# Performance work log

Measured on AMD Instinct MI355X. Metric: run time of the kernel, lower is better.

Reference implementation:

```python
import jax, jax.numpy as jnp
from jax import lax
import numpy as np

N_ENT = 50000
N_REL = 500
E = 800000
H = 128
BS = 1024
C = 96
KER = 7
KH, KW = 8, 16  # H = KH*KW
TOPK = 15
FLAT = C * (2 * KH - KER + 1) * (KW - KER + 1)  # 96*10*10 = 9600


def mlp3(x, w0, b0, w1, b1, w2, b2):
    x = jax.nn.relu(x @ w0 + b0)
    x = jax.nn.relu(x @ w1 + b1)
    return x @ w2 + b2


def compute_corr(x1, x2):
    x1 = x1 - jnp.mean(x1, 0, keepdims=True)
    x2 = x2 - jnp.mean(x2, 0, keepdims=True)
    s1 = jnp.sqrt(jnp.mean(x1 * x1))
    s2 = jnp.sqrt(jnp.mean(x2 * x2))
    return jnp.abs(jnp.mean(x1 * x2)) / (s1 * s2)


def comp_layer(node_emb, rel_emb, src, dst, rel_id, neigh_w):
    # CompGCN 'mul' composition: u_mul_e
    comp = node_emb[src] * rel_emb[rel_id]                      # (E,H)
    score = jnp.sum(comp * node_emb[dst], axis=-1)              # e_dot_v, (E,)
    # edge softmax over incoming edges of each dst node
    m = jax.ops.segment_max(score, dst, num_segments=N_ENT)
    e = jnp.exp(score - m[dst])
    z = jax.ops.segment_sum(e, dst, num_segments=N_ENT)
    norm = e / z[dst]                                           # (E,)
    # select_topk: keep top-15 in-edges per dst by norm
    order = jnp.lexsort((-norm, dst))                           # sort by dst, then norm desc
    deg = jax.ops.segment_sum(jnp.ones((E,), jnp.int32), dst, num_segments=N_ENT)
    start = jnp.cumsum(deg) - deg                               # group start per node
    rank = jnp.arange(E, dtype=jnp.int32) - start[dst[order]]
    keep = jnp.zeros((E,), bool).at[order].set(rank < TOPK)
    w = norm * keep                                             # weighted, pruned
    # copy_e + sum aggregation to dst
    neigh = jax.ops.segment_sum(comp * w[:, None], dst, num_segments=N_ENT)
    return jnp.tanh(neigh @ neigh_w)


def conve(head, rel, ent_emb, conv_w, conv_b, fc_w, fc_b, score_b):
    x = jnp.concatenate([head.reshape(-1, 1, KH, KW), rel.reshape(-1, 1, KH, KW)], axis=2)  # (bs,1,16,16)
    x = lax.conv_general_dilated(x, conv_w, (1, 1), 'VALID') + conv_b[None, :, None, None]
    x = jax.nn.relu(x).reshape(x.shape[0], -1)                  # (bs,FLAT)
    x = jax.nn.relu(x @ fc_w + fc_b)                            # (bs,H)
    return jax.nn.sigmoid(x @ ent_emb.T + score_b)              # (bs,N_ENT)


def setup_inputs() -> dict:
    key = jax.random.key(0)
    ks = jax.random.split(key, 24)
    def g(i, shape, scale=0.05):
        return jax.random.normal(ks[i], shape, jnp.float32) * scale
    return dict(
        h_id=jax.random.randint(ks[0], (BS,), 0, N_ENT),
        r_id=jax.random.randint(ks[1], (BS,), 0, 2 * N_REL),
        src=jax.random.randint(ks[2], (E,), 0, N_ENT),
        dst=jax.random.randint(ks[3], (E,), 0, N_ENT),
        rel_id=jax.random.randint(ks[4], (E,), 0, 2 * N_REL),
        ent_emb=g(5, (N_ENT, H)),
        rel_emb0=g(6, (2 * N_REL, H)),
        neigh_w=g(7, (H, H)),
        S_w=g(8, (H, H)), S_b=jnp.zeros((H,), jnp.float32),
        L_w=g(9, (H, H)), L_b=jnp.zeros((H,), jnp.float32),
        pred_rel_emb=g(10, (2 * N_REL, H)),
        phi_w0=g(11, (H, 200)), phi_b0=jnp.zeros((200,), jnp.float32),
        phi_w1=g(12, (200, 200)), phi_b1=jnp.zeros((200,), jnp.float32),
        phi_w2=g(13, (200, 1)), phi_b2=jnp.zeros((1,), jnp.float32),
        psi_w0=g(14, (H, 200)), psi_b0=jnp.zeros((200,), jnp.float32),
        psi_w1=g(15, (200, 200)), psi_b1=jnp.zeros((200,), jnp.float32),
        psi_w2=g(16, (200, 1)), psi_b2=jnp.zeros((1,), jnp.float32),
        conv_w=g(17, (C, 1, KER, KER)), conv_b=jnp.zeros((C,), jnp.float32),
        fc_w=g(18, (FLAT, H)), fc_b=jnp.zeros((H,), jnp.float32),
        score_b=jnp.zeros((N_ENT,), jnp.float32),
    )


def reference(h_id, r_id, src, dst, rel_id,
              ent_emb, rel_emb0, neigh_w, S_w, S_b, L_w, L_b, pred_rel_emb,
              phi_w0, phi_b0, phi_w1, phi_b1, phi_w2, phi_b2,
              psi_w0, psi_b0, psi_w1, psi_b1, psi_w2, psi_b2,
              conv_w, conv_b, fc_w, fc_b, score_b):
    common = ent_emb @ S_w + S_b
    private = ent_emb @ L_w + L_b
    c1 = comp_layer(common, rel_emb0, src, dst, rel_id, neigh_w)
    c2 = comp_layer(private, rel_emb0, src, dst, rel_id, neigh_w)
    ent_out = ent_emb + c1 + c2
    corr = compute_corr(mlp3(c1, phi_w0, phi_b0, phi_w1, phi_b1, phi_w2, phi_b2),
                        mlp3(c2, psi_w0, psi_b0, psi_w1, psi_b1, psi_w2, psi_b2))
    head = ent_out[h_id]
    rel = pred_rel_emb[r_id]
    score = conve(head, rel, ent_out, conv_w, conv_b, fc_w, fc_b, score_b)
    return (score, corr)
```

## Files before the change

### kernel.cpp

```cpp
#include <hip/hip_runtime.h>
#include <math.h>

typedef unsigned short ushort;
typedef unsigned int   uint;
typedef short bf16x8 __attribute__((ext_vector_type(8)));
typedef float f32x4  __attribute__((ext_vector_type(4)));
typedef ushort u16x8 __attribute__((ext_vector_type(8)));
typedef ushort u16x4 __attribute__((ext_vector_type(4)));

#define N_ENTS   50000
#define E_EDGES  800000
#define HD       128
#define BSZ      1024
#define C_CH     96
#define FLATD    9600
#define TOPK_K   15
#define HIDD     200
#define SPLITK   10
#define OUT_SCORE ((size_t)BSZ * N_ENTS)

#define MPAD     50048
#define NPAD_ENT 50176
#define KPAD200  224
#define NPAD200  256
#define L2E      1.4426950408889634f

#define OFF_EP       ((size_t)0)
#define OFF_ENTOUT   ((size_t)25624576)
#define OFF_RELBF    ((size_t)38469632)
#define OFF_PRELBF   ((size_t)38725632)
#define OFF_SWT      ((size_t)38981632)
#define OFF_LWT      ((size_t)39014400)
#define OFF_NWT      ((size_t)39047168)
#define OFF_P0T      ((size_t)39079936)
#define OFF_Q0T      ((size_t)39145472)
#define OFF_P1T      ((size_t)39211008)
#define OFF_Q1T      ((size_t)39325696)
#define OFF_FCT      ((size_t)39440384)
#define OFF_SC       ((size_t)41897984)
#define OFF_W        ((size_t)48297984)
#define OFF_SIDX     ((size_t)54697984)
#define OFF_EORD     ((size_t)67497984)
#define OFF_DEG      ((size_t)70697984)
#define OFF_START    ((size_t)70897984)
#define OFF_CUR      ((size_t)71097984)
#define OFF_BSUM     ((size_t)71297984)
#define OFF_X1       ((size_t)71302080)
#define OFF_X2       ((size_t)71502080)
#define OFF_RED      ((size_t)71702080)
#define OFF_XFC      ((size_t)71702336)
#define OFF_ARENA    ((size_t)71964480)

__device__ inline ushort f2b(float f) {
    uint u = __float_as_uint(f);
    return (ushort)((u + 0x7fffu + ((u >> 16) & 1u)) >> 16);
}
__device__ inline float b2f(ushort u) { return __uint_as_float((uint)u << 16); }
__device__ inline float fexp2(float x) { return __builtin_amdgcn_exp2f(x); }
__device__ inline float frcp(float x)  { return __builtin_amdgcn_rcpf(x); }
__device__ inline float fsigmoid(float x) { return frcp(1.f + fexp2(-x * L2E)); }
__device__ inline float ftanh(float x) {
    float ax = fabsf(x);
    float t = fexp2(ax * (-2.f * L2E));
    float r = (1.f - t) * frcp(1.f + t);
    return copysignf(r, x);
}

__global__ void k_cvt(const float* __restrict__ in, ushort* __restrict__ out,
                      int M, int Mpad, int K) {
    int i = blockIdx.x * 256 + threadIdx.x;
    if (i >= Mpad * K) return;
    int r = i / K;
    out[i] = (r < M) ? f2b(in[i]) : (ushort)0;
}

__global__ void k_cvt2(const float* __restrict__ in0, ushort* __restrict__ out0,
                       const float* __restrict__ in1, ushort* __restrict__ out1, int n) {
    const float* in = blockIdx.z ? in1 : in0;
    ushort* out = blockIdx.z ? out1 : out0;
    int i = blockIdx.x * 256 + threadIdx.x;
    if (i < n) out[i] = f2b(in[i]);
}

__global__ __launch_bounds__(256) void k_tcvtT(const float* __restrict__ in, ushort* __restrict__ out,
                                               int K, int N, int Kpad, int Npad) {
    __shared__ float t[32][33];
    int k0 = blockIdx.x * 32, n0 = blockIdx.y * 32;
    int tx = threadIdx.x & 31, ty = threadIdx.x >> 5;
    for (int i = ty; i < 32; i += 8) {
        int k = k0 + i, n = n0 + tx;
        t[i][tx] = (k < K && n < N) ? in[(size_t)k * N + n] : 0.f;
    }
    __syncthreads();
    for (int i = ty; i < 32; i += 8) {
        int n = n0 + i, k = k0 + tx;
        if (n < Npad && k < Kpad) out[(size_t)n * Kpad + k] = f2b(t[tx][i]);
    }
}

__global__ __launch_bounds__(256) void k_tcvt7(
    const float* __restrict__ S_w, const float* __restrict__ L_w, const float* __restrict__ n_w,
    const float* __restrict__ p0, const float* __restrict__ q0,
    const float* __restrict__ p1, const float* __restrict__ q1,
    ushort* __restrict__ Swt, ushort* __restrict__ Lwt, ushort* __restrict__ nWt,
    ushort* __restrict__ p0t, ushort* __restrict__ q0t,
    ushort* __restrict__ p1t, ushort* __restrict__ q1t) {
    const float* in; ushort* out; int K, N, Kp, Np;
    switch (blockIdx.z) {
        case 0: in = S_w; out = Swt; K = 128; N = 128; Kp = 128; Np = 128; break;
        case 1: in = L_w; out = Lwt; K = 128; N = 128; Kp = 128; Np = 128; break;
        case 2: in = n_w; out = nWt; K = 128; N = 128; Kp = 128; Np = 128; break;
        case 3: in = p0;  out = p0t; K = 128; N = HIDD; Kp = 128; Np = NPAD200; break;
        case 4: in = q0;  out = q0t; K = 128; N = HIDD; Kp = 128; Np = NPAD200; break;
        case 5: in = p1;  out = p1t; K = HIDD; N = HIDD; Kp = KPAD200; Np = NPAD200; break;
        default: in = q1; out = q1t; K = HIDD; N = HIDD; Kp = KPAD200; Np = NPAD200; break;
    }
    __shared__ float t[32][33];
    int k0 = blockIdx.x * 32, n0 = blockIdx.y * 32;
    if (k0 >= Kp || n0 >= Np) return;
    int tx = threadIdx.x & 31, ty = threadIdx.x >> 5;
    for (int i = ty; i < 32; i += 8) {
        int k = k0 + i, n = n0 + tx;
        t[i][tx] = (k < K && n < N) ? in[(size_t)k * N + n] : 0.f;
    }
    __syncthreads();
    for (int i = ty; i < 32; i += 8) {
        int n = n0 + i, k = k0 + tx;
        if (n < Np && k < Kp) out[(size_t)n * Kp + k] = f2b(t[tx][i]);
    }
}

template <int WM, int WN, int OUTBF, int FUSE2>
__global__ __launch_bounds__(256) void k_mgemm(
    const ushort* __restrict__ A, int lda,
    const ushort* __restrict__ Bt, int ldb,
    const float* __restrict__ bias, void* __restrict__ Cout, int ldc,
    int M, int N, int K, int kChunk, int epi, int iofs, int npad,
    const ushort* __restrict__ A2, const ushort* __restrict__ Bt2,
    const float* __restrict__ bias2, void* __restrict__ Cout2, int iofs2) {
    if (FUSE2 && blockIdx.z == 1) { A = A2; Bt = Bt2; bias = bias2; Cout = Cout2; iofs = iofs2; }
    const int w = threadIdx.x >> 6, lane = threadIdx.x & 63;
    const int wr = w / WN, wc = w % WN;
    const int row0 = blockIdx.x * (WM * 64) + wr * 64;
    const int col0 = blockIdx.y * (WN * 64) + wc * 64;
    const int lr = lane & 15;
    const int kg = (lane >> 4) * 8;
    const int kb = FUSE2 ? 0 : blockIdx.z * kChunk;
    const int ke = kb + kChunk;

    f32x4 acc[4][4];
#pragma unroll
    for (int i = 0; i < 4; i++)
#pragma unroll
        for (int j = 0; j < 4; j++) acc[i][j] = (f32x4){0.f, 0.f, 0.f, 0.f};

    for (int kk = kb; kk < ke; kk += 32) {
        bf16x8 af[4], bfr[4];
#pragma unroll
        for (int i = 0; i < 4; i++) {
            int r = row0 + i * 16 + lr;
            r = min(r, M - 1);
            af[i] = *(const bf16x8*)(A + (size_t)r * lda + kk + kg);
        }
#pragma unroll
        for (int j = 0; j < 4; j++) {
            int c = col0 + j * 16 + lr;
            bfr[j] = *(const bf16x8*)(Bt + (size_t)c * ldb + kk + kg);
        }
#pragma unroll
        for (int i = 0; i < 4; i++)
#pragma unroll
            for (int j = 0; j < 4; j++)
                acc[i][j] = __builtin_amdgcn_mfma_f32_16x16x32_bf16(af[i], bfr[j], acc[i][j], 0, 0, 0);
    }

    const int cr = (lane >> 4) * 4, cc = lane & 15;
    if (!FUSE2 && gridDim.z > 1) {
        float* P = (float*)Cout + (size_t)blockIdx.z * M * ldc;
#pragma unroll
        for (int i = 0; i < 4; i++)
#pragma unroll
            for (int j = 0; j < 4; j++) {
                int col = col0 + j * 16 + cc;
                if (col >= N) continue;
#pragma unroll
                for (int t = 0; t < 4; t++) {
                    int row = row0 + i * 16 + cr + t;
                    if (row < M) P[(size_t)row * ldc + col] = acc[i][j][t];
                }
            }
    } else {
#pragma unroll
        for (int i = 0; i < 4; i++)
#pragma unroll
            for (int j = 0; j < 4; j++) {
                int col = col0 + j * 16 + cc;
                if (col >= (OUTBF ? npad : N)) continue;
                bool valid = col < N;
                float bi = (bias && valid) ? bias[col] : 0.f;
#pragma unroll
                for (int t = 0; t < 4; t++) {
                    int row = row0 + i * 16 + cr + t;
                    if (row >= M) continue;
                    float v = acc[i][j][t] + bi;
                    if (epi == 1) v = fmaxf(v, 0.f);
                    else if (epi == 2) v = ftanh(v);
                    else if (epi == 3) v = fsigmoid(v);
                    if (!valid) v = 0.f;
                    if (OUTBF) {
                        size_t idx = (iofs < 0) ? ((size_t)row * ldc + col)
                                   : ((size_t)row * ldc + ((size_t)(col >> 1) << 2) + (col & 1) + iofs);
                        ((ushort*)Cout)[idx] = f2b(v);
                    } else {
                        ((float*)Cout)[(size_t)row * ldc + col] = v;
                    }
                }
            }
    }
}

__global__ __launch_bounds__(256) void k_score(
    const ushort* __restrict__ A,
    const ushort* __restrict__ Bt,
    const float* __restrict__ bias,
    float* __restrict__ C, int N) {
    __shared__ __align__(16) float st[4][16][68];
    const int w = threadIdx.x >> 6, lane = threadIdx.x & 63;
    const int lr = lane & 15, kg = (lane >> 4) * 8;
    const int cr = (lane >> 4) * 4, cc = lane & 15;
    int flat = blockIdx.y * 16 + blockIdx.x;
    int swz = (flat & 7) * 392 + (flat >> 3);
    const int row0 = (swz & 15) * 64;
    const int colw = (swz >> 4) * 256 + w * 64;

    f32x4 acc[4][4];
#pragma unroll
    for (int i = 0; i < 4; i++)
#pragma unroll
        for (int j = 0; j < 4; j++) acc[i][j] = (f32x4){0.f, 0.f, 0.f, 0.f};

    for (int kk = 0; kk < HD; kk += 32) {
        bf16x8 af[4], bfr[4];
#pragma unroll
        for (int i = 0; i < 4; i++)
            af[i] = *(const bf16x8*)(A + (size_t)(row0 + i * 16 + lr) * HD + kk + kg);
#pragma unroll
        for (int j = 0; j < 4; j++)
            bfr[j] = *(const bf16x8*)(Bt + (size_t)(colw + j * 16 + lr) * HD + kk + kg);
#pragma unroll
        for (int i = 0; i < 4; i++)
#pragma unroll
            for (int j = 0; j < 4; j++)
                acc[i][j] = __builtin_amdgcn_mfma_f32_16x16x32_bf16(af[i], bfr[j], acc[i][j], 0, 0, 0);
    }

#pragma unroll
    for (int i = 0; i < 4; i++) {
#pragma unroll
        for (int j = 0; j < 4; j++) {
            int col = colw + j * 16 + cc;
            float bi = (col < N) ? bias[col] : 0.f;
#pragma unroll
            for (int t = 0; t < 4; t++)
                st[w][cr + t][j * 16 + cc] = fsigmoid(acc[i][j][t] + bi);
        }
#pragma unroll
        for (int p = 0; p < 4; p++) {
            int r = p * 4 + (lane >> 4);
            int cq = (lane & 15) * 4;
            float4 v = *(const float4*)&st[w][r][cq];
            int gc = colw + cq;
            if (gc < N)
                *(float4*)&C[(size_t)(row0 + i * 16 + r) * N + gc] = v;
        }
    }
}

__global__ __launch_bounds__(256) void k_mlp2(
    const ushort* __restrict__ A0, const ushort* __restrict__ W0t0,
    const float* __restrict__ b00, const ushort* __restrict__ W1t0,
    const float* __restrict__ b10, const float* __restrict__ w20,
    const float* __restrict__ b20, float* __restrict__ xo0,
    const ushort* __restrict__ A1, const ushort* __restrict__ W0t1,
    const float* __restrict__ b01, const ushort* __restrict__ W1t1,
    const float* __restrict__ b11, const float* __restrict__ w21,
    const float* __restrict__ b21, float* __restrict__ xo1) {
    const ushort* A   = blockIdx.z ? A1 : A0;
    const ushort* W0t = blockIdx.z ? W0t1 : W0t0;
    const float*  b0  = blockIdx.z ? b01 : b00;
    const ushort* W1t = blockIdx.z ? W1t1 : W1t0;
    const float*  b1  = blockIdx.z ? b11 : b10;
    const float*  w2  = blockIdx.z ? w21 : w20;
    const float*  b2  = blockIdx.z ? b21 : b20;
    float*        x   = blockIdx.z ? xo1 : xo0;

    __shared__ __align__(16) char lbuf[64 * 232 * 2];
    __shared__ float w2e[256], b1e[256], b0e[256];
    const int tid = threadIdx.x;
    const int w = tid >> 6, lane = tid & 63;
    const int lr = lane & 15, kg = (lane >> 4) * 8;
    const int cr = (lane >> 4) * 4, cc = lane & 15;
    const int row0 = blockIdx.x * 64;
    {
        int c = tid;
        w2e[c] = (c < HIDD) ? w2[c] : 0.f;
        b1e[c] = (c < HIDD) ? b1[c] : 0.f;
        b0e[c] = (c < HIDD) ? b0[c] : 0.f;
    }
    __syncthreads();
    ushort* g1 = (ushort*)lbuf;

    f32x4 acc[4][4];
#pragma unroll
    for (int i = 0; i < 4; i++)
#pragma unroll
        for (int j = 0; j < 4; j++) acc[i][j] = (f32x4){0.f, 0.f, 0.f, 0.f};
    for (int kk = 0; kk < 128; kk += 32) {
        bf16x8 af[4], bfr[4];
#pragma unroll
        for (int i = 0; i < 4; i++)
            af[i] = *(const bf16x8*)(A + (size_t)(row0 + i * 16 + lr) * HD + kk + kg);
#pragma unroll
        for (int j = 0; j < 4; j++)
            bfr[j] = *(const bf16x8*)(W0t + (size_t)(w * 64 + j * 16 + lr) * 128 + kk + kg);
#pragma unroll
        for (int i = 0; i < 4; i++)
#pragma unroll
            for (int j = 0; j < 4; j++)
                acc[i][j] = __builtin_amdgcn_mfma_f32_16x16x32_bf16(af[i], bfr[j], acc[i][j], 0, 0, 0);
    }
#pragma unroll
    for (int i = 0; i < 4; i++)
#pragma unroll
        for (int j = 0; j < 4; j++) {
            int col = w * 64 + j * 16 + cc;
            if (col < KPAD200) {
                float bi = b0e[col];
#pragma unroll
                for (int t = 0; t < 4; t++)
                    g1[(i * 16 + cr + t) * 232 + col] = f2b(fmaxf(acc[i][j][t] + bi, 0.f));
            }
        }
    __syncthreads();

    f32x4 a2[4][4];
#pragma unroll
    for (int i = 0; i < 4; i++)
#pragma unroll
        for (int j = 0; j < 4; j++) a2[i][j] = (f32x4){0.f, 0.f, 0.f, 0.f};
    for (int ks = 0; ks < 7; ks++) {
        int kk = ks * 32;
        bf16x8 af[4], bfr[4];
#pragma unroll
        for (int i = 0; i < 4; i++)
            af[i] = *(const bf16x8*)(g1 + (i * 16 + lr) * 232 + kk + kg);
#pragma unroll
        for (int j = 0; j < 4; j++)
            bfr[j] = *(const bf16x8*)(W1t + (size_t)(w * 64 + j * 16 + lr) * KPAD200 + kk + kg);
#pragma unroll
        for (int i = 0; i < 4; i++)
#pragma unroll
            for (int j = 0; j < 4; j++)
                a2[i][j] = __builtin_amdgcn_mfma_f32_16x16x32_bf16(af[i], bfr[j], a2[i][j], 0, 0, 0);
    }
    __syncthreads();

    float* pbuf = (float*)lbuf;
#pragma unroll
    for (int i = 0; i < 4; i++)
#pragma unroll
        for (int t = 0; t < 4; t++) {
            float s = 0.f;
#pragma unroll
            for (int j = 0; j < 4; j++) {
                int col = w * 64 + j * 16 + cc;
                s += fmaxf(a2[i][j][t] + b1e[col], 0.f) * w2e[col];
            }
            pbuf[(i * 16 + cr + t) * 65 + w * 16 + cc] = s;
        }
    __syncthreads();
    if (tid < 64) {
        float s = b2[0];
        for (int q = 0; q < 64; q++) s += pbuf[tid * 65 + q];
        int gr = row0 + tid;
        if (gr < N_ENTS) x[gr] = s;
    }
}

__global__ void k_deg(const int* __restrict__ dst, int* __restrict__ deg) {
    int e = blockIdx.x * 256 + threadIdx.x;
    if (e < E_EDGES) atomicAdd(&deg[dst[e]], 1);
}

__global__ void k_scan1(const int* __restrict__ in, int* __restrict__ out,
                        int* __restrict__ bsum, int n) {
    __shared__ int sh[256];
    int i = blockIdx.x * 256 + threadIdx.x;
    int v = (i < n) ? in[i] : 0;
    sh[threadIdx.x] = v; __syncthreads();
    for (int off = 1; off < 256; off <<= 1) {
        int t = (threadIdx.x >= off) ? sh[threadIdx.x - off] : 0;
        __syncthreads();
        sh[threadIdx.x] += t;
        __syncthreads();
    }
    if (i < n) out[i] = sh[threadIdx.x] - v;
    if (threadIdx.x == 255) bsum[blockIdx.x] = sh[255];
}

__global__ void k_scan2(int* __restrict__ bsum, int nb) {
    __shared__ int sh[1024];
    int t = threadIdx.x;
    int v = (t < nb) ? bsum[t] : 0;
    sh[t] = v; __syncthreads();
    for (int off = 1; off < 1024; off <<= 1) {
        int u = (t >= off) ? sh[t - off] : 0;
        __syncthreads();
        sh[t] += u;
        __syncthreads();
    }
    if (t < nb) bsum[t] = sh[t] - v;
}

__global__ void k_scan3(int* __restrict__ out, const int* __restrict__ bsum, int n) {
    int i = blockIdx.x * 256 + threadIdx.x;
    if (i < n) out[i] += bsum[blockIdx.x];
}

__global__ void k_scatter(const int* __restrict__ dst, const int* __restrict__ start,
                          int* __restrict__ cursor, int* __restrict__ eorder) {
    int e = blockIdx.x * 256 + threadIdx.x;
    if (e < E_EDGES) {
        int n = dst[e];
        int p = start[n] + atomicAdd(&cursor[n], 1);
        eorder[p] = e;
    }
}

__global__ void k_mkidx(const int* __restrict__ eorder, const int* __restrict__ src,
                        const int* __restrict__ dst, const int* __restrict__ rel_id,
                        int4* __restrict__ sidx) {
    int slot = blockIdx.x * 256 + threadIdx.x;
    if (slot < E_EDGES) {
        int e = eorder[slot];
        sidx[slot] = make_int4(src[e], dst[e], rel_id[e], e);
    }
}

__global__ __launch_bounds__(256) void k_scores(
    const int4* __restrict__ sidx, const ushort* __restrict__ ep,
    const ushort* __restrict__ rel, float2* __restrict__ sc) {
    int gg = threadIdx.x >> 3, l = threadIdx.x & 7;
    int slot = blockIdx.x * 32 + gg;
    int4 si = sidx[slot];
    const ushort* rs = ep + (size_t)si.x * 256 + l * 32;
    const ushort* rd = ep + (size_t)si.y * 256 + l * 32;
    const ushort* rr = rel + (size_t)si.z * 128 + l * 16;
    u16x8 sv[4], dv[4], rv[2];
#pragma unroll
    for (int i = 0; i < 4; i++) sv[i] = *(const u16x8*)(rs + 8 * i);
#pragma unroll
    for (int i = 0; i < 4; i++) dv[i] = *(const u16x8*)(rd + 8 * i);
#pragma unroll
    for (int i = 0; i < 2; i++) rv[i] = *(const u16x8*)(rr + 8 * i);
    float a = 0.f, b = 0.f;
#pragma unroll
    for (int Q = 0; Q < 8; Q++) {
        int G = Q >> 1, k = (Q & 1) * 4;
        float r0 = b2f(rv[Q >> 2][(Q & 3) * 2]);
        float r1 = b2f(rv[Q >> 2][(Q & 3) * 2 + 1]);
        a += b2f(sv[G][k])     * r0 * b2f(dv[G][k])     + b2f(sv[G][k + 1]) * r1 * b2f(dv[G][k + 1]);
        b += b2f(sv[G][k + 2]) * r0 * b2f(dv[G][k + 2]) + b2f(sv[G][k + 3]) * r1 * b2f(dv[G][k + 3]);
    }
#pragma unroll
    for (int m = 4; m; m >>= 1) { a += __shfl_xor(a, m, 8); b += __shfl_xor(b, m, 8); }
    if (l == 0) sc[slot] = make_float2(a, b);
}

__global__ __launch_bounds__(256) void k_softtop(
    const int* __restrict__ start, const int* __restrict__ deg,
    const int4* __restrict__ sidx, const float2* __restrict__ sc, float2* __restrict__ w) {
    int n = blockIdx.x * 16 + (threadIdx.x >> 4);
    int l = threadIdx.x & 15;
    if (n >= N_ENTS) return;
    int b = start[n], d = deg[n];
    if (d == 0) return;
    float m1 = -INFINITY, m2 = -INFINITY;
    for (int i = l; i < d; i += 16) {
        float2 s = sc[b + i];
        m1 = fmaxf(m1, s.x); m2 = fmaxf(m2, s.y);
    }
#pragma unroll
    for (int o = 8; o; o >>= 1) { m1 = fmaxf(m1, __shfl_xor(m1, o, 16)); m2 = fmaxf(m2, __shfl_xor(m2, o, 16)); }
    float z1 = 0.f, z2 = 0.f;
    for (int i = l; i < d; i += 16) {
        float2 s = sc[b + i];
        z1 += fexp2((s.x - m1) * L2E); z2 += fexp2((s.y - m2) * L2E);
    }
#pragma unroll
    for (int o = 8; o; o >>= 1) { z1 += __shfl_xor(z1, o, 16); z2 += __shfl_xor(z2, o, 16); }
    float iz1 = frcp(z1), iz2 = frcp(z2);
    for (int i = l; i < d; i += 16) {
        float2 sp = sc[b + i];
        int ei = sidx[b + i].w;
        int r1 = 0, r2 = 0;
        for (int j = 0; j < d; j++) {
            float2 sq = sc[b + j];
            int ej = sidx[b + j].w;
            r1 += (sq.x > sp.x) || (sq.x == sp.x && ej < ei);
            r2 += (sq.y > sp.y) || (sq.y == sp.y && ej < ei);
        }
        w[b + i] = make_float2(r1 < TOPK_K ? fexp2((sp.x - m1) * L2E) * iz1 : 0.f,
                               r2 < TOPK_K ? fexp2((sp.y - m2) * L2E) * iz2 : 0.f);
    }
}

__global__ __launch_bounds__(256) void k_agg(
    const int4* __restrict__ sidx, const int* __restrict__ start, const int* __restrict__ deg,
    const float2* __restrict__ w, const ushort* __restrict__ ep, const ushort* __restrict__ rel,
    ushort* __restrict__ neigh1, ushort* __restrict__ neigh2) {
    __shared__ float4 part[3][64];
    int n = blockIdx.x;
    int wid = threadIdx.x >> 6, g = threadIdx.x & 63;
    int b = start[n], end = b + deg[n];
    float2 a1 = make_float2(0.f, 0.f), a2 = make_float2(0.f, 0.f);
    float2 c1 = make_float2(0.f, 0.f), c2 = make_float2(0.f, 0.f);
    for (int s = b + wid; s < end; s += 8) {
        int sB = s + 4;
        bool hB = sB < end;
        int4 siA = sidx[s];
        float2 wA = w[s];
        int4 siB = hB ? sidx[sB] : siA;
        float2 wB = hB ? w[sB] : make_float2(0.f, 0.f);
        u16x4 vA = *(const u16x4*)(ep + (size_t)siA.x * 256 + g * 4);
        uint  rA = *(const uint*)(rel + (size_t)siA.z * 128 + g * 2);
        u16x4 vB = *(const u16x4*)(ep + (size_t)siB.x * 256 + g * 4);
        uint  rB = *(const uint*)(rel + (size_t)siB.z * 128 + g * 2);
        float rAx = b2f((ushort)(rA & 0xffffu)), rAy = b2f((ushort)(rA >> 16));
        a1.x += wA.x * b2f(vA[0]) * rAx;  a1.y += wA.x * b2f(vA[1]) * rAy;
        a2.x += wA.y * b2f(vA[2]) * rAx;  a2.y += wA.y * b2f(vA[3]) * rAy;
        float rBx = b2f((ushort)(rB & 0xffffu)), rBy = b2f((ushort)(rB >> 16));
        c1.x += wB.x * b2f(vB[0]) * rBx;  c1.y += wB.x * b2f(vB[1]) * rBy;
        c2.x += wB.y * b2f(vB[2]) * rBx;  c2.y += wB.y * b2f(vB[3]) * rBy;
    }
    a1.x += c1.x; a1.y += c1.y; a2.x += c2.x; a2.y += c2.y;
    if (wid > 0) part[wid - 1][g] = make_float4(a1.x, a1.y, a2.x, a2.y);
    __syncthreads();
    if (wid == 0) {
#pragma unroll
        for (int k = 0; k < 3; k++) {
            float4 p = part[k][g];
            a1.x += p.x; a1.y += p.y; a2.x += p.z; a2.y += p.w;
        }
        uint o1 = (uint)f2b(a1.x) | ((uint)f2b(a1.y) << 16);
        uint o2 = (uint)f2b(a2.x) | ((uint)f2b(a2.y) << 16);
        ((uint*)(neigh1 + (size_t)n * HD))[g] = o1;
        ((uint*)(neigh2 + (size_t)n * HD))[g] = o2;
    }
}

__global__ void k_entout(const float* __restrict__ ent, const ushort* __restrict__ c1,
                         const ushort* __restrict__ c2, ushort* __restrict__ out) {
    int i = blockIdx.x * 256 + threadIdx.x;
    if (i >= NPAD_ENT * HD) return;
    int r = i >> 7;
    float v = 0.f;
    if (r < N_ENTS) v = ent[i] + b2f(c1[i]) + b2f(c2[i]);
    out[i] = (r < N_ENTS) ? f2b(v) : (ushort)0;
}

__global__ void k_corr1(const float* __restrict__ x1, const float* __restrict__ x2,
                        float* __restrict__ red) {
    __shared__ float sa[1024], sb[1024];
    int t = threadIdx.x;
    float s1 = 0.f, s2 = 0.f;
    for (int i = t; i < N_ENTS; i += 1024) { s1 += x1[i]; s2 += x2[i]; }
    sa[t] = s1; sb[t] = s2; __syncthreads();
    for (int o = 512; o > 0; o >>= 1) {
        if (t < o) { sa[t] += sa[t + o]; sb[t] += sb[t + o]; }
        __syncthreads();
    }
    if (t == 0) { red[0] = sa[0] / (float)N_ENTS; red[1] = sb[0] / (float)N_ENTS; }
}

__global__ void k_corr2(const float* __restrict__ x1, const float* __restrict__ x2,
                        const float* __restrict__ red, float* __restrict__ out) {
    __shared__ float s11[1024], s22[1024], s12[1024];
    int t = threadIdx.x;
    float m1 = red[0], m2 = red[1];
    float a11 = 0.f, a22 = 0.f, a12 = 0.f;
    for (int i = t; i < N_ENTS; i += 1024) {
        float a = x1[i] - m1, b = x2[i] - m2;
        a11 += a * a; a22 += b * b; a12 += a * b;
    }
    s11[t] = a11; s22[t] = a22; s12[t] = a12; __syncthreads();
    for (int o = 512; o > 0; o >>= 1) {
        if (t < o) { s11[t] += s11[t + o]; s22[t] += s22[t + o]; s12[t] += s12[t + o]; }
        __syncthreads();
    }
    if (t == 0) {
        float v11 = s11[0] / (float)N_ENTS, v22 = s22[0] / (float)N_ENTS, v12 = s12[0] / (float)N_ENTS;
        out[0] = fabsf(v12) / (sqrtf(v11) * sqrtf(v22));
    }
}

__global__ void k_conv(const int* __restrict__ h_id, const int* __restrict__ r_id,
                       const ushort* __restrict__ entout, const ushort* __restrict__ prel,
                       const float* __restrict__ cw, const float* __restrict__ cb,
                       ushort* __restrict__ out) {
    __shared__ float img[256];
    __shared__ float filt[C_CH * 49];
    int b = blockIdx.x, tid = threadIdx.x;
    if (tid < 128) img[tid] = b2f(entout[(size_t)h_id[b] * HD + tid]);
    else           img[tid] = b2f(prel[(size_t)r_id[b] * HD + (tid - 128)]);
    for (int i = tid; i < C_CH * 49; i += 256) filt[i] = cw[i];
    __syncthreads();
    for (int idx = tid; idx < FLATD; idx += 256) {
        int o = idx / 100, rem = idx % 100, i = rem / 10, j = rem % 10;
        float acc = cb[o];
        const float* f = &filt[o * 49];
#pragma unroll
        for (int ki = 0; ki < 7; ki++)
#pragma unroll
            for (int kj = 0; kj < 7; kj++)
                acc += img[(i + ki) * 16 + (j + kj)] * f[ki * 7 + kj];
        out[(size_t)b * FLATD + idx] = f2b(fmaxf(acc, 0.f));
    }
}

__global__ void k_fcreduce(const float* __restrict__ part, const float* __restrict__ bias,
                           ushort* __restrict__ out) {
    int i = blockIdx.x * 256 + threadIdx.x;
    if (i >= BSZ * HD) return;
    float s = 0.f;
    for (int z = 0; z < SPLITK; z++) s += part[(size_t)z * BSZ * HD + i];
    s += bias[i & (HD - 1)];
    out[i] = f2b(fmaxf(s, 0.f));
}

extern "C" void kernel_launch(void* const* d_in, const int* in_sizes, int n_in,
                              void* d_out, int out_size, void* d_ws, size_t ws_size,
                              hipStream_t stream) {
    const int* h_id    = (const int*)d_in[0];
    const int* r_id    = (const int*)d_in[1];
    const int* src     = (const int*)d_in[2];
    const int* dst     = (const int*)d_in[3];
    const int* rel_id  = (const int*)d_in[4];
    const float* ent_emb  = (const float*)d_in[5];
    const float* rel_emb0 = (const float*)d_in[6];
    const float* neigh_w  = (const float*)d_in[7];
    const float* S_w = (const float*)d_in[8];
    const float* S_b = (const float*)d_in[9];
    const float* L_w = (const float*)d_in[10];
    const float* L_b = (const float*)d_in[11];
    const float* pred_rel = (const float*)d_in[12];
    const float* phi_w0 = (const float*)d_in[13]; const float* phi_b0 = (const float*)d_in[14];
    const float* phi_w1 = (const float*)d_in[15]; const float* phi_b1 = (const float*)d_in[16];
    const float* phi_w2 = (const float*)d_in[17]; const float* phi_b2 = (const float*)d_in[18];
    const float* psi_w0 = (const float*)d_in[19]; const float* psi_b0 = (const float*)d_in[20];
    const float* psi_w1 = (const float*)d_in[21]; const float* psi_b1 = (const float*)d_in[22];
    const float* psi_w2 = (const float*)d_in[23]; const float* psi_b2 = (const float*)d_in[24];
    const float* conv_w = (const float*)d_in[25]; const float* conv_b = (const float*)d_in[26];
    const float* fc_w   = (const float*)d_in[27]; const float* fc_b   = (const float*)d_in[28];
    const float* score_b= (const float*)d_in[29];

    char* base = (char*)d_ws;
    ushort* ep       = (ushort*)(base + OFF_EP);
    ushort* entout_bf= (ushort*)(base + OFF_ENTOUT);
    ushort* rel_bf   = (ushort*)(base + OFF_RELBF);
    ushort* prel_bf  = (ushort*)(base + OFF_PRELBF);
    ushort* Swt      = (ushort*)(base + OFF_SWT);
    ushort* Lwt      = (ushort*)(base + OFF_LWT);
    ushort* nWt      = (ushort*)(base + OFF_NWT);
    ushort* p0t      = (ushort*)(base + OFF_P0T);
    ushort* q0t      = (ushort*)(base + OFF_Q0T);
    ushort* p1t      = (ushort*)(base + OFF_P1T);
    ushort* q1t      = (ushort*)(base + OFF_Q1T);
    ushort* fct      = (ushort*)(base + OFF_FCT);
    float2* sc       = (float2*)(base + OFF_SC);
    float2* wpair    = (float2*)(base + OFF_W);
    int4*   sidx     = (int4*)(base + OFF_SIDX);
    int*    eorder   = (int*)(base + OFF_EORD);
    int*    deg      = (int*)(base + OFF_DEG);
    int*    startp   = (int*)(base + OFF_START);
    int*    cursor   = (int*)(base + OFF_CUR);
    int*    bsum     = (int*)(base + OFF_BSUM);
    float*  x1       = (float*)(base + OFF_X1);
    float*  x2       = (float*)(base + OFF_X2);
    float*  red      = (float*)(base + OFF_RED);
    ushort* xfc_bf   = (ushort*)(base + OFF_XFC);
    ushort* c1_bf    = (ushort*)(base + OFF_EP);
    ushort* c2_bf    = (ushort*)(base + OFF_EP + 12812288);
    ushort* ent_bf   = (ushort*)(base + OFF_ARENA);
    ushort* neigh1_bf= (ushort*)(base + OFF_ARENA);
    ushort* neigh2_bf= (ushort*)(base + OFF_ARENA + 12812288);
    ushort* convout  = (ushort*)(base + OFF_ARENA);
    float*  fcpart   = (float*)(base + OFF_ARENA + 22421504);
    float*  outf     = (float*)d_out;

    k_cvt<<<dim3((MPAD * HD + 255) / 256), 256, 0, stream>>>(ent_emb, ent_bf, N_ENTS, MPAD, HD);
    k_cvt2<<<dim3(500, 1, 2), 256, 0, stream>>>(rel_emb0, rel_bf, pred_rel, prel_bf, 1000 * HD);
    k_tcvt7<<<dim3(7, 8, 7), 256, 0, stream>>>(S_w, L_w, neigh_w, phi_w0, psi_w0, phi_w1, psi_w1,
                                               Swt, Lwt, nWt, p0t, q0t, p1t, q1t);
    k_tcvtT<<<dim3(300, 4), 256, 0, stream>>>(fc_w, fct, FLATD, 128, FLATD, 128);

    k_mgemm<2,2,1,1><<<dim3(391, 1, 2), 256, 0, stream>>>(
        ent_bf, HD, Swt, HD, S_b, ep, 256, N_ENTS, HD, HD, HD, 0, 0, HD,
        ent_bf, Lwt, L_b, ep, 2);

    hipMemsetAsync(deg, 0, N_ENTS * sizeof(int), stream);
    hipMemsetAsync(cursor, 0, N_ENTS * sizeof(int), stream);
    k_deg<<<dim3((E_EDGES + 255) / 256), 256, 0, stream>>>(dst, deg);
    int nscan = (N_ENTS + 255) / 256;
    k_scan1<<<dim3(nscan), 256, 0, stream>>>(deg, startp, bsum, N_ENTS);
    k_scan2<<<dim3(1), 1024, 0, stream>>>(bsum, nscan);
    k_scan3<<<dim3(nscan), 256, 0, stream>>>(startp, bsum, N_ENTS);
    k_scatter<<<dim3((E_EDGES + 255) / 256), 256, 0, stream>>>(dst, startp, cursor, eorder);
    k_mkidx<<<dim3((E_EDGES + 255) / 256), 256, 0, stream>>>(eorder, src, dst, rel_id, sidx);

    k_scores<<<dim3(E_EDGES / 32), 256, 0, stream>>>(sidx, ep, rel_bf, sc);
    k_softtop<<<dim3((N_ENTS + 15) / 16), 256, 0, stream>>>(startp, deg, sidx, sc, wpair);
    k_agg<<<dim3(N_ENTS), 256, 0, stream>>>(sidx, startp, deg, wpair, ep, rel_bf,
                                            neigh1_bf, neigh2_bf);

    k_mgemm<2,2,1,1><<<dim3(391, 1, 2), 256, 0, stream>>>(
        neigh1_bf, HD, nWt, HD, nullptr, c1_bf, HD, N_ENTS, HD, HD, HD, 2, -1, HD,
        neigh2_bf, nWt, nullptr, c2_bf, -1);

    k_entout<<<dim3((NPAD_ENT * HD + 255) / 256), 256, 0, stream>>>(ent_emb, c1_bf, c2_bf, entout_bf);

    k_mlp2<<<dim3(MPAD / 64, 1, 2), 256, 0, stream>>>(
        c1_bf, p0t, phi_b0, p1t, phi_b1, phi_w2, phi_b2, x1,
        c2_bf, q0t, psi_b0, q1t, psi_b1, psi_w2, psi_b2, x2);

    k_corr1<<<dim3(1), 1024, 0, stream>>>(x1, x2, red);
    k_corr2<<<dim3(1), 1024, 0, stream>>>(x1, x2, red, outf + OUT_SCORE);

    k_conv<<<dim3(BSZ), 256, 0, stream>>>(h_id, r_id, entout_bf, prel_bf, conv_w, conv_b, convout);
    k_mgemm<2,2,0,0><<<dim3(8, 1, SPLITK), 256, 0, stream>>>(
        convout, FLATD, fct, FLATD, nullptr, fcpart, HD, BSZ, HD, FLATD, FLATD / SPLITK, 0, -1, HD,
        nullptr, nullptr, nullptr, nullptr, 0);
    k_fcreduce<<<dim3((BSZ * HD + 255) / 256), 256, 0, stream>>>(fcpart, fc_b, xfc_bf);

    k_score<<<dim3(16, 196), 256, 0, stream>>>(xfc_bf, entout_bf, score_b, outf, N_ENTS);
}
```

Baseline: 699.4 us.

## Fuse neigh GEMM with ent_out, merge scatter/mkidx and corr kernels, tune agg

Several independent changes. The tanh GEMM for both branches is fused with the ent_out sum into one kernel, scatter and index building are merged, and the two corr kernels are combined, which removes launches and intermediate round-trips. k_score uses nontemporal stores for the large output, k_scores changes its load pattern, k_softtop skips top-k ranking for nodes with degree at most 15, and k_agg unrolls to four edges per iteration for more memory-level parallelism. entout padding rows beyond N_ENTS are no longer zeroed, which may matter if the score GEMM reads padded rows.

```diff
diff --git a/kernel.cpp b/kernel.cpp
--- a/kernel.cpp
+++ b/kernel.cpp
@@ -40,7 +40,6 @@
 #define OFF_SC       ((size_t)41897984)
 #define OFF_W        ((size_t)48297984)
 #define OFF_SIDX     ((size_t)54697984)
-#define OFF_EORD     ((size_t)67497984)
 #define OFF_DEG      ((size_t)70697984)
 #define OFF_START    ((size_t)70897984)
 #define OFF_CUR      ((size_t)71097984)
@@ -219,11 +218,65 @@
     }
 }
 
+__global__ __launch_bounds__(256) void k_tanh2ent(
+    const ushort* __restrict__ neigh1, const ushort* __restrict__ neigh2,
+    const ushort* __restrict__ nWt, const float* __restrict__ ent,
+    ushort* __restrict__ c1o, ushort* __restrict__ c2o, ushort* __restrict__ eo) {
+    const int w = threadIdx.x >> 6, lane = threadIdx.x & 63;
+    const int wr = w >> 1, wc = w & 1;
+    const int row0 = blockIdx.x * 128 + wr * 64;
+    const int col0 = wc * 64;
+    const int lr = lane & 15, kg = (lane >> 4) * 8;
+
+    f32x4 a1[4][4], a2[4][4];
+#pragma unroll
+    for (int i = 0; i < 4; i++)
+#pragma unroll
+        for (int j = 0; j < 4; j++) { a1[i][j] = (f32x4){0,0,0,0}; a2[i][j] = (f32x4){0,0,0,0}; }
+
+    for (int kk = 0; kk < HD; kk += 32) {
+        bf16x8 f1[4], f2v[4], bfr[4];
+#pragma unroll
+        for (int i = 0; i < 4; i++) {
+            int r = min(row0 + i * 16 + lr, N_ENTS - 1);
+            f1[i]  = *(const bf16x8*)(neigh1 + (size_t)r * HD + kk + kg);
+            f2v[i] = *(const bf16x8*)(neigh2 + (size_t)r * HD + kk + kg);
+        }
+#pragma unroll
+        for (int j = 0; j < 4; j++)
+            bfr[j] = *(const bf16x8*)(nWt + (size_t)(col0 + j * 16 + lr) * HD + kk + kg);
+#pragma unroll
+        for (int i = 0; i < 4; i++)
+#pragma unroll
+            for (int j = 0; j < 4; j++) {
+                a1[i][j] = __builtin_amdgcn_mfma_f32_16x16x32_bf16(f1[i],  bfr[j], a1[i][j], 0, 0, 0);
+                a2[i][j] = __builtin_amdgcn_mfma_f32_16x16x32_bf16(f2v[i], bfr[j], a2[i][j], 0, 0, 0);
+            }
+    }
+
+    const int cr = (lane >> 4) * 4, cc = lane & 15;
+#pragma unroll
+    for (int i = 0; i < 4; i++)
+#pragma unroll
+        for (int j = 0; j < 4; j++) {
+            int col = col0 + j * 16 + cc;
+#pragma unroll
+            for (int t = 0; t < 4; t++) {
+                int row = row0 + i * 16 + cr + t;
+                if (row >= N_ENTS) continue;
+                float t1 = ftanh(a1[i][j][t]);
+                float t2 = ftanh(a2[i][j][t]);
+                size_t idx = (size_t)row * HD + col;
+                c1o[idx] = f2b(t1);
+                c2o[idx] = f2b(t2);
+                eo[idx] = f2b(ent[idx] + t1 + t2);
+            }
+        }
+}
+
 __global__ __launch_bounds__(256) void k_score(
-    const ushort* __restrict__ A,
-    const ushort* __restrict__ Bt,
-    const float* __restrict__ bias,
-    float* __restrict__ C, int N) {
+    const ushort* __restrict__ A, const ushort* __restrict__ Bt,
+    const float* __restrict__ bias, float* __restrict__ C, int N) {
     __shared__ __align__(16) float st[4][16][68];
     const int w = threadIdx.x >> 6, lane = threadIdx.x & 63;
     const int lr = lane & 15, kg = (lane >> 4) * 8;
@@ -268,10 +321,10 @@
         for (int p = 0; p < 4; p++) {
             int r = p * 4 + (lane >> 4);
             int cq = (lane & 15) * 4;
-            float4 v = *(const float4*)&st[w][r][cq];
+            f32x4 v = *(const f32x4*)&st[w][r][cq];
             int gc = colw + cq;
             if (gc < N)
-                *(float4*)&C[(size_t)(row0 + i * 16 + r) * N + gc] = v;
+                __builtin_nontemporal_store(v, (f32x4*)&C[(size_t)(row0 + i * 16 + r) * N + gc]);
         }
     }
 }
@@ -427,23 +480,14 @@
     if (i < n) out[i] += bsum[blockIdx.x];
 }
 
-__global__ void k_scatter(const int* __restrict__ dst, const int* __restrict__ start,
-                          int* __restrict__ cursor, int* __restrict__ eorder) {
+__global__ void k_scatter2(const int* __restrict__ src, const int* __restrict__ dst,
+                           const int* __restrict__ rel_id, const int* __restrict__ start,
+                           int* __restrict__ cursor, int4* __restrict__ sidx) {
     int e = blockIdx.x * 256 + threadIdx.x;
     if (e < E_EDGES) {
         int n = dst[e];
         int p = start[n] + atomicAdd(&cursor[n], 1);
-        eorder[p] = e;
-    }
-}
-
-__global__ void k_mkidx(const int* __restrict__ eorder, const int* __restrict__ src,
-                        const int* __restrict__ dst, const int* __restrict__ rel_id,
-                        int4* __restrict__ sidx) {
-    int slot = blockIdx.x * 256 + threadIdx.x;
-    if (slot < E_EDGES) {
-        int e = eorder[slot];
-        sidx[slot] = make_int4(src[e], dst[e], rel_id[e], e);
+        sidx[p] = make_int4(src[e], n, rel_id[e], e);
     }
 }
 
@@ -453,24 +497,27 @@
     int gg = threadIdx.x >> 3, l = threadIdx.x & 7;
     int slot = blockIdx.x * 32 + gg;
     int4 si = sidx[slot];
-    const ushort* rs = ep + (size_t)si.x * 256 + l * 32;
-    const ushort* rd = ep + (size_t)si.y * 256 + l * 32;
-    const ushort* rr = rel + (size_t)si.z * 128 + l * 16;
-    u16x8 sv[4], dv[4], rv[2];
-#pragma unroll
-    for (int i = 0; i < 4; i++) sv[i] = *(const u16x8*)(rs + 8 * i);
-#pragma unroll
-    for (int i = 0; i < 4; i++) dv[i] = *(const u16x8*)(rd + 8 * i);
-#pragma unroll
-    for (int i = 0; i < 2; i++) rv[i] = *(const u16x8*)(rr + 8 * i);
+    const ushort* rs = ep + (size_t)si.x * 256;
+    const ushort* rd = ep + (size_t)si.y * 256;
+    const ushort* rr = rel + (size_t)si.z * 128;
+    u16x8 sv[4], dv[4];
+    uint2 rv[4];
+#pragma unroll
+    for (int i = 0; i < 4; i++) {
+        int t = i * 8 + l;
+        sv[i] = *(const u16x8*)(rs + t * 8);
+        dv[i] = *(const u16x8*)(rd + t * 8);
+        rv[i] = *(const uint2*)(rr + t * 4);
+    }
     float a = 0.f, b = 0.f;
 #pragma unroll
-    for (int Q = 0; Q < 8; Q++) {
-        int G = Q >> 1, k = (Q & 1) * 4;
-        float r0 = b2f(rv[Q >> 2][(Q & 3) * 2]);
-        float r1 = b2f(rv[Q >> 2][(Q & 3) * 2 + 1]);
-        a += b2f(sv[G][k])     * r0 * b2f(dv[G][k])     + b2f(sv[G][k + 1]) * r1 * b2f(dv[G][k + 1]);
-        b += b2f(sv[G][k + 2]) * r0 * b2f(dv[G][k + 2]) + b2f(sv[G][k + 3]) * r1 * b2f(dv[G][k + 3]);
+    for (int i = 0; i < 4; i++) {
+        float r0 = b2f((ushort)(rv[i].x & 0xffffu)), r1 = b2f((ushort)(rv[i].x >> 16));
+        float r2 = b2f((ushort)(rv[i].y & 0xffffu)), r3 = b2f((ushort)(rv[i].y >> 16));
+        a += b2f(sv[i][0]) * r0 * b2f(dv[i][0]) + b2f(sv[i][1]) * r1 * b2f(dv[i][1])
+           + b2f(sv[i][4]) * r2 * b2f(dv[i][4]) + b2f(sv[i][5]) * r3 * b2f(dv[i][5]);
+        b += b2f(sv[i][2]) * r0 * b2f(dv[i][2]) + b2f(sv[i][3]) * r1 * b2f(dv[i][3])
+           + b2f(sv[i][6]) * r2 * b2f(dv[i][6]) + b2f(sv[i][7]) * r3 * b2f(dv[i][7]);
     }
 #pragma unroll
     for (int m = 4; m; m >>= 1) { a += __shfl_xor(a, m, 8); b += __shfl_xor(b, m, 8); }
@@ -500,6 +547,14 @@
 #pragma unroll
     for (int o = 8; o; o >>= 1) { z1 += __shfl_xor(z1, o, 16); z2 += __shfl_xor(z2, o, 16); }
     float iz1 = frcp(z1), iz2 = frcp(z2);
+    if (d <= TOPK_K) {
+        for (int i = l; i < d; i += 16) {
+            float2 sp = sc[b + i];
+            w[b + i] = make_float2(fexp2((sp.x - m1) * L2E) * iz1,
+                                   fexp2((sp.y - m2) * L2E) * iz2);
+        }
+        return;
+    }
     for (int i = l; i < d; i += 16) {
         float2 sp = sc[b + i];
         int ei = sidx[b + i].w;
@@ -523,27 +578,42 @@
     int n = blockIdx.x;
     int wid = threadIdx.x >> 6, g = threadIdx.x & 63;
     int b = start[n], end = b + deg[n];
-    float2 a1 = make_float2(0.f, 0.f), a2 = make_float2(0.f, 0.f);
-    float2 c1 = make_float2(0.f, 0.f), c2 = make_float2(0.f, 0.f);
-    for (int s = b + wid; s < end; s += 8) {
-        int sB = s + 4;
-        bool hB = sB < end;
+    float2 p1a = {0.f, 0.f}, p2a = {0.f, 0.f}, p1b = {0.f, 0.f}, p2b = {0.f, 0.f};
+    for (int s = b + wid; s < end; s += 16) {
+        int sB = s + 4, sC = s + 8, sD = s + 12;
+        bool hB = sB < end, hC = sC < end, hD = sD < end;
         int4 siA = sidx[s];
+        int4 siB = hB ? sidx[sB] : siA;
+        int4 siC = hC ? sidx[sC] : siA;
+        int4 siD = hD ? sidx[sD] : siA;
         float2 wA = w[s];
-        int4 siB = hB ? sidx[sB] : siA;
         float2 wB = hB ? w[sB] : make_float2(0.f, 0.f);
+        float2 wC = hC ? w[sC] : make_float2(0.f, 0.f);
+        float2 wD = hD ? w[sD] : make_float2(0.f, 0.f);
         u16x4 vA = *(const u16x4*)(ep + (size_t)siA.x * 256 + g * 4);
-        uint  rA = *(const uint*)(rel + (size_t)siA.z * 128 + g * 2);
         u16x4 vB = *(const u16x4*)(ep + (size_t)siB.x * 256 + g * 4);
-        uint  rB = *(const uint*)(rel + (size_t)siB.z * 128 + g * 2);
-        float rAx = b2f((ushort)(rA & 0xffffu)), rAy = b2f((ushort)(rA >> 16));
-        a1.x += wA.x * b2f(vA[0]) * rAx;  a1.y += wA.x * b2f(vA[1]) * rAy;
-        a2.x += wA.y * b2f(vA[2]) * rAx;  a2.y += wA.y * b2f(vA[3]) * rAy;
-        float rBx = b2f((ushort)(rB & 0xffffu)), rBy = b2f((ushort)(rB >> 16));
-        c1.x += wB.x * b2f(vB[0]) * rBx;  c1.y += wB.x * b2f(vB[1]) * rBy;
-        c2.x += wB.y * b2f(vB[2]) * rBx;  c2.y += wB.y * b2f(vB[3]) * rBy;
-    }
-    a1.x += c1.x; a1.y += c1.y; a2.x += c2.x; a2.y += c2.y;
+        u16x4 vC = *(const u16x4*)(ep + (size_t)siC.x * 256 + g * 4);
+        u16x4 vD = *(const u16x4*)(ep + (size_t)siD.x * 256 + g * 4);
+        uint rA = *(const uint*)(rel + (size_t)siA.z * 128 + g * 2);
+        uint rB = *(const uint*)(rel + (size_t)siB.z * 128 + g * 2);
+        uint rC = *(const uint*)(rel + (size_t)siC.z * 128 + g * 2);
+        uint rD = *(const uint*)(rel + (size_t)siD.z * 128 + g * 2);
+        float rx, ry;
+        rx = b2f((ushort)(rA & 0xffffu)); ry = b2f((ushort)(rA >> 16));
+        p1a.x += wA.x * b2f(vA[0]) * rx;  p1a.y += wA.x * b2f(vA[1]) * ry;
+        p2a.x += wA.y * b2f(vA[2]) * rx;  p2a.y += wA.y * b2f(vA[3]) * ry;
+        rx = b2f((ushort)(rB & 0xffffu)); ry = b2f((ushort)(rB >> 16));
+        p1b.x += wB.x * b2f(vB[0]) * rx;  p1b.y += wB.x * b2f(vB[1]) * ry;
+        p2b.x += wB.y * b2f(vB[2]) * rx;  p2b.y += wB.y * b2f(vB[3]) * ry;
+        rx = b2f((ushort)(rC & 0xffffu)); ry = b2f((ushort)(rC >> 16));
+        p1a.x += wC.x * b2f(vC[0]) * rx;  p1a.y += wC.x * b2f(vC[1]) * ry;
+        p2a.x += wC.y * b2f(vC[2]) * rx;  p2a.y += wC.y * b2f(vC[3]) * ry;
+        rx = b2f((ushort)(rD & 0xffffu)); ry = b2f((ushort)(rD >> 16));
+        p1b.x += wD.x * b2f(vD[0]) * rx;  p1b.y += wD.x * b2f(vD[1]) * ry;
+        p2b.x += wD.y * b2f(vD[2]) * rx;  p2b.y += wD.y * b2f(vD[3]) * ry;
+    }
+    float2 a1 = make_float2(p1a.x + p1b.x, p1a.y + p1b.y);
+    float2 a2 = make_float2(p2a.x + p2b.x, p2a.y + p2b.y);
     if (wid > 0) part[wid - 1][g] = make_float4(a1.x, a1.y, a2.x, a2.y);
     __syncthreads();
     if (wid == 0) {
@@ -559,19 +629,9 @@
     }
 }
 
-__global__ void k_entout(const float* __restrict__ ent, const ushort* __restrict__ c1,
-                         const ushort* __restrict__ c2, ushort* __restrict__ out) {
-    int i = blockIdx.x * 256 + threadIdx.x;
-    if (i >= NPAD_ENT * HD) return;
-    int r = i >> 7;
-    float v = 0.f;
-    if (r < N_ENTS) v = ent[i] + b2f(c1[i]) + b2f(c2[i]);
-    out[i] = (r < N_ENTS) ? f2b(v) : (ushort)0;
-}
-
-__global__ void k_corr1(const float* __restrict__ x1, const float* __restrict__ x2,
-                        float* __restrict__ red) {
-    __shared__ float sa[1024], sb[1024];
+__global__ void k_corr(const float* __restrict__ x1, const float* __restrict__ x2,
+                       float* __restrict__ out) {
+    __shared__ float sa[1024], sb[1024], sc_[1024];
     int t = threadIdx.x;
     float s1 = 0.f, s2 = 0.f;
     for (int i = t; i < N_ENTS; i += 1024) { s1 += x1[i]; s2 += x2[i]; }
@@ -580,26 +640,20 @@
         if (t < o) { sa[t] += sa[t + o]; sb[t] += sb[t + o]; }
         __syncthreads();
     }
-    if (t == 0) { red[0] = sa[0] / (float)N_ENTS; red[1] = sb[0] / (float)N_ENTS; }
-}
-
-__global__ void k_corr2(const float* __restrict__ x1, const float* __restrict__ x2,
-                        const float* __restrict__ red, float* __restrict__ out) {
-    __shared__ float s11[1024], s22[1024], s12[1024];
-    int t = threadIdx.x;
-    float m1 = red[0], m2 = red[1];
+    float m1 = sa[0] / (float)N_ENTS, m2 = sb[0] / (float)N_ENTS;
+    __syncthreads();
     float a11 = 0.f, a22 = 0.f, a12 = 0.f;
     for (int i = t; i < N_ENTS; i += 1024) {
         float a = x1[i] - m1, b = x2[i] - m2;
         a11 += a * a; a22 += b * b; a12 += a * b;
     }
-    s11[t] = a11; s22[t] = a22; s12[t] = a12; __syncthreads();
+    sa[t] = a11; sb[t] = a22; sc_[t] = a12; __syncthreads();
     for (int o = 512; o > 0; o >>= 1) {
-        if (t < o) { s11[t] += s11[t + o]; s22[t] += s22[t + o]; s12[t] += s12[t + o]; }
+        if (t < o) { sa[t] += sa[t + o]; sb[t] += sb[t + o]; sc_[t] += sc_[t + o]; }
         __syncthreads();
     }
     if (t == 0) {
-        float v11 = s11[0] / (float)N_ENTS, v22 = s22[0] / (float)N_ENTS, v12 = s12[0] / (float)N_ENTS;
+        float v11 = sa[0] / (float)N_ENTS, v22 = sb[0] / (float)N_ENTS, v12 = sc_[0] / (float)N_ENTS;
         out[0] = fabsf(v12) / (sqrtf(v11) * sqrtf(v22));
     }
 }
@@ -680,14 +734,12 @@
     float2* sc       = (float2*)(base + OFF_SC);
     float2* wpair    = (float2*)(base + OFF_W);
     int4*   sidx     = (int4*)(base + OFF_SIDX);
-    int*    eorder   = (int*)(base + OFF_EORD);
     int*    deg      = (int*)(base + OFF_DEG);
     int*    startp   = (int*)(base + OFF_START);
     int*    cursor   = (int*)(base + OFF_CUR);
     int*    bsum     = (int*)(base + OFF_BSUM);
     float*  x1       = (float*)(base + OFF_X1);
     float*  x2       = (float*)(base + OFF_X2);
-    float*  red      = (float*)(base + OFF_RED);
     ushort* xfc_bf   = (ushort*)(base + OFF_XFC);
     ushort* c1_bf    = (ushort*)(base + OFF_EP);
     ushort* c2_bf    = (ushort*)(base + OFF_EP + 12812288);
@@ -715,26 +767,21 @@
     k_scan1<<<dim3(nscan), 256, 0, stream>>>(deg, startp, bsum, N_ENTS);
     k_scan2<<<dim3(1), 1024, 0, stream>>>(bsum, nscan);
     k_scan3<<<dim3(nscan), 256, 0, stream>>>(startp, bsum, N_ENTS);
-    k_scatter<<<dim3((E_EDGES + 255) / 256), 256, 0, stream>>>(dst, startp, cursor, eorder);
-    k_mkidx<<<dim3((E_EDGES + 255) / 256), 256, 0, stream>>>(eorder, src, dst, rel_id, sidx);
+    k_scatter2<<<dim3((E_EDGES + 255) / 256), 256, 0, stream>>>(src, dst, rel_id, startp, cursor, sidx);
 
     k_scores<<<dim3(E_EDGES / 32), 256, 0, stream>>>(sidx, ep, rel_bf, sc);
     k_softtop<<<dim3((N_ENTS + 15) / 16), 256, 0, stream>>>(startp, deg, sidx, sc, wpair);
     k_agg<<<dim3(N_ENTS), 256, 0, stream>>>(sidx, startp, deg, wpair, ep, rel_bf,
                                             neigh1_bf, neigh2_bf);
 
-    k_mgemm<2,2,1,1><<<dim3(391, 1, 2), 256, 0, stream>>>(
-        neigh1_bf, HD, nWt, HD, nullptr, c1_bf, HD, N_ENTS, HD, HD, HD, 2, -1, HD,
-        neigh2_bf, nWt, nullptr, c2_bf, -1);
-
-    k_entout<<<dim3((NPAD_ENT * HD + 255) / 256), 256, 0, stream>>>(ent_emb, c1_bf, c2_bf, entout_bf);
+    k_tanh2ent<<<dim3(391), 256, 0, stream>>>(neigh1_bf, neigh2_bf, nWt, ent_emb,
+                                              c1_bf, c2_bf, entout_bf);
 
     k_mlp2<<<dim3(MPAD / 64, 1, 2), 256, 0, stream>>>(
         c1_bf, p0t, phi_b0, p1t, phi_b1, phi_w2, phi_b2, x1,
         c2_bf, q0t, psi_b0, q1t, psi_b1, psi_w2, psi_b2, x2);
 
-    k_corr1<<<dim3(1), 1024, 0, stream>>>(x1, x2, red);
-    k_corr2<<<dim3(1), 1024, 0, stream>>>(x1, x2, red, outf + OUT_SCORE);
+    k_corr<<<dim3(1), 1024, 0, stream>>>(x1, x2, outf + OUT_SCORE);
 
     k_conv<<<dim3(BSZ), 256, 0, stream>>>(h_id, r_id, entout_bf, prel_bf, conv_w, conv_b, convout);
     k_mgemm<2,2,0,0><<<dim3(8, 1, SPLITK), 256, 0, stream>>>(
```

Result: faster. 649.7 us (-7.1%).
